# Optimization experiments

Hardware: AMD Instinct MI355X
Metric: run time of the kernel (lower is better)

Reference implementation:

```python
import jax, jax.numpy as jnp
import numpy as np

B, H, W = 4, 1024, 1024

# 8-tap Sobel-style stencil: offsets in (u, v) units of (dx, dy)
OFF_U = jnp.array([-1.0, -1.0, -1.0, 0.0, 0.0, 1.0, 1.0, 1.0], dtype=jnp.float32)
OFF_V = jnp.array([-1.0, 0.0, 1.0, -1.0, 1.0, -1.0, 0.0, 1.0], dtype=jnp.float32)
KU = jnp.array([-0.25, -0.5, -0.25, 0.0, 0.0, 0.25, 0.5, 0.25], dtype=jnp.float32)
KV = jnp.array([-0.25, 0.0, 0.25, -0.5, 0.5, -0.25, 0.0, 0.25], dtype=jnp.float32)


def setup_inputs() -> dict:
    key = jax.random.key(0)
    k1, k2 = jax.random.split(key)
    x = jax.random.uniform(k1, (B, 3, H, W), dtype=jnp.float32)
    sigma = jax.random.uniform(k2, (B,), dtype=jnp.float32) * 2.0 + 0.5  # pixels
    return {"x": x, "sigma": sigma}


def _bilinear(tex, u, v):
    # tex: [3, H, W]; u, v: [8, H, W] normalized UV in [0,1]
    Hh, Ww = tex.shape[1], tex.shape[2]
    px = u * Ww - 0.5
    py = v * Hh - 0.5
    x0 = jnp.floor(px)
    y0 = jnp.floor(py)
    fx = (px - x0)[None]  # [1,8,H,W]
    fy = (py - y0)[None]
    x0i = jnp.clip(x0.astype(jnp.int32), 0, Ww - 1)
    x1i = jnp.clip(x0i + 1, 0, Ww - 1)
    y0i = jnp.clip(y0.astype(jnp.int32), 0, Hh - 1)
    y1i = jnp.clip(y0i + 1, 0, Hh - 1)
    t00 = tex[:, y0i, x0i]  # [3,8,H,W]
    t01 = tex[:, y0i, x1i]
    t10 = tex[:, y1i, x0i]
    t11 = tex[:, y1i, x1i]
    return (t00 * (1 - fx) * (1 - fy) + t01 * fx * (1 - fy)
            + t10 * (1 - fx) * fy + t11 * fx * fy)


def reference(x, sigma):
    Bb, C, Hh, Ww = x.shape
    ys, xs = jnp.meshgrid(jnp.arange(Hh, dtype=x.dtype),
                          jnp.arange(Ww, dtype=x.dtype), indexing='ij')
    u0 = (xs + 0.5) / Ww  # pixel-center UV
    v0 = (ys + 0.5) / Hh
    dx = sigma / Ww  # [B]
    dy = sigma / Hh
    u = u0[None, None] + OFF_U[None, :, None, None] * dx[:, None, None, None]  # [B,8,H,W]
    v = v0[None, None] + OFF_V[None, :, None, None] * dy[:, None, None, None]
    s = jax.vmap(_bilinear)(x, u, v)  # [B,3,8,H,W]
    s_u = jnp.einsum('bcthw,t->bchw', s, KU)
    s_v = jnp.einsum('bcthw,t->bchw', s, KV)
    lum = jnp.array([100.0, 1.0, 1.0], dtype=x.dtype)[None, :, None, None]
    s_u = s_u * lum
    s_v = s_v * lum
    # structure tensor components E, G, F
    return jnp.stack([(s_u * s_u).sum(1), (s_v * s_v).sum(1), (s_u * s_v).sum(1)], axis=1)
```

## Files before the change

### kernel.cpp

```cpp
#include <hip/hip_runtime.h>


#define W_ 1024
#define H_ 1024
#define PLANE (1 << 20)
#define TCOLS 256
#define TROWS 8
#define ROWS 8
#define LSTRIDE 264
#define GPR 66

__device__ __forceinline__ float lerp1(float a, float b, float f) {
    return fmaf(f, b - a, a);
}

__device__ __forceinline__ void async_copy16(const float* g, float* s) {
    __builtin_amdgcn_global_load_lds(
        (const __attribute__((address_space(1))) unsigned int*)g,
        (__attribute__((address_space(3))) unsigned int*)s,
        16, 0, 0);
}

__device__ void slow_pixel(const float* __restrict__ Xb, float* __restrict__ Ob,
                           float sg, int xi, int y)
{
    float imf = floorf(-sg), ipf = floorf(sg);
    float fm  = -sg - imf;
    float fp  =  sg - ipf;
    int   im  = (int)imf, ip = (int)ipf;

    int cm0 = min(max(xi + im, 0), W_ - 1), cm1 = min(cm0 + 1, W_ - 1);
    int cp0 = min(max(xi + ip, 0), W_ - 1), cp1 = min(cp0 + 1, W_ - 1);
    int rm0 = min(max(y + im, 0), H_ - 1),  rm1 = min(rm0 + 1, H_ - 1);
    int rp0 = min(max(y + ip, 0), H_ - 1),  rp1 = min(rp0 + 1, H_ - 1);

    int o_rm0 = rm0 << 10, o_rm1 = rm1 << 10;
    int o_rp0 = rp0 << 10, o_rp1 = rp1 << 10;
    int o_r0  = y   << 10;

    float oxx = 0.f, oyy = 0.f, oxy = 0.f;

    #pragma unroll
    for (int c = 0; c < 3; ++c) {
        const float* base = Xb + ((size_t)c << 20);

        float hm_m0 = lerp1(base[o_rm0 + cm0], base[o_rm0 + cm1], fm);
        float hm_m1 = lerp1(base[o_rm1 + cm0], base[o_rm1 + cm1], fm);
        float hm_0  = lerp1(base[o_r0  + cm0], base[o_r0  + cm1], fm);
        float hm_p0 = lerp1(base[o_rp0 + cm0], base[o_rp0 + cm1], fm);
        float hm_p1 = lerp1(base[o_rp1 + cm0], base[o_rp1 + cm1], fm);
        float hp_m0 = lerp1(base[o_rm0 + cp0], base[o_rm0 + cp1], fp);
        float hp_m1 = lerp1(base[o_rm1 + cp0], base[o_rm1 + cp1], fp);
        float hp_0  = lerp1(base[o_r0  + cp0], base[o_r0  + cp1], fp);
        float hp_p0 = lerp1(base[o_rp0 + cp0], base[o_rp0 + cp1], fp);
        float hp_p1 = lerp1(base[o_rp1 + cp0], base[o_rp1 + cp1], fp);
        float h0_m0 = base[o_rm0 + xi], h0_m1 = base[o_rm1 + xi];
        float h0_p0 = base[o_rp0 + xi], h0_p1 = base[o_rp1 + xi];

        float t0 = lerp1(hm_m0, hm_m1, fm);
        float t1 = hm_0;
        float t2 = lerp1(hm_p0, hm_p1, fp);
        float t3 = lerp1(h0_m0, h0_m1, fm);
        float t4 = lerp1(h0_p0, h0_p1, fp);
        float t5 = lerp1(hp_m0, hp_m1, fm);
        float t6 = hp_0;
        float t7 = lerp1(hp_p0, hp_p1, fp);

        float su = 0.25f * (t5 + t7 - t0 - t2) + 0.5f * (t6 - t1);
        float sv = 0.25f * (t2 + t7 - t0 - t5) + 0.5f * (t4 - t3);

        float l2 = (c == 0) ? 10000.f : 1.f;
        oxx = fmaf(l2 * su, su, oxx);
        oyy = fmaf(l2 * sv, sv, oyy);
        oxy = fmaf(l2 * su, sv, oxy);
    }

    int pix = (y << 10) | xi;
    Ob[pix]             = oxx;
    Ob[PLANE + pix]     = oyy;
    Ob[2 * PLANE + pix] = oxy;
}

template<int N>
__device__ __forceinline__ void acc(float (&arr)[N], int k, float val) {
    if (k >= 0 && k < N) arr[k] += val;
}

template<int IP>
__device__ void fast_tile(const float* __restrict__ Xb, float* __restrict__ Ob,
                          float fp, float fm, int x0, int y0,
                          int tx, float* smem)
{
    constexpr int LROWS  = TROWS + 2 * IP + 2;
    constexpr int RW     = ROWS + 2 * IP + 2;
    constexpr int NG     = 3 * LROWS * GPR;
    constexpr int FULLIT = NG / 256;

    int x = x0 + tx;

    auto stage = [&](int g) {
        int row  = g / GPR;
        int grp  = g - row * GPR;
        int c    = row / LROWS;
        int lrow = row - c * LROWS;
        int gr   = min(max(y0 - IP - 1 + lrow, 0), H_ - 1);
        int gc   = min(max(x0 - 4 + grp * 4, 0), W_ - 4);
        async_copy16(Xb + ((size_t)c << 20) + (gr << 10) + gc,
                     smem + g * 4);
    };

    #pragma unroll
    for (int it = 0; it < FULLIT; ++it)
        stage(it * 256 + tx);
    if (FULLIT * 256 + tx < NG)
        stage(FULLIT * 256 + tx);

    __syncthreads();

    float oxx[ROWS], oyy[ROWS], oxy[ROWS];
    #pragma unroll
    for (int k = 0; k < ROWS; ++k) { oxx[k] = 0.f; oyy[k] = 0.f; oxy[k] = 0.f; }

    const float* spb = smem + tx + (3 - IP);

    #pragma unroll
    for (int c = 0; c < 3; ++c) {
        const float* sp = spb + c * (LROWS * LSTRIDE);

        float su[ROWS], sv[ROWS];
        #pragma unroll
        for (int k = 0; k < ROWS; ++k) { su[k] = 0.f; sv[k] = 0.f; }

        #pragma unroll
        for (int w = 0; w < RW; ++w) {
            float a0 = sp[w * LSTRIDE];
            float a1 = sp[w * LSTRIDE + 1];
            float cc = sp[w * LSTRIDE + IP + 1];
            float b0 = sp[w * LSTRIDE + 2 * IP + 1];
            float b1 = sp[w * LSTRIDE + 2 * IP + 2];
            float hm = lerp1(a0, a1, fm);
            float hp = lerp1(b0, b1, fp);
            float q  = hp - hm;
            float A  = 0.25f * q;
            float hq = 0.5f  * q;
            float Bv = fmaf(0.25f, hm + hp, 0.5f * cc);
            float fpA = fp * A,  fmA = fm * A;
            float fpB = fp * Bv, fmB = fm * Bv;

            acc(su, w,              fpA);
            acc(su, w - 1,          fmA);
            acc(su, w - IP - 1,     hq);
            acc(su, w - 2*IP - 1,   fmA);
            acc(su, w - 2*IP - 2,   fpA);
            acc(sv, w,             -fpB);
            acc(sv, w - 1,         -fmB);
            acc(sv, w - 2*IP - 1,   fmB);
            acc(sv, w - 2*IP - 2,   fpB);
        }

        float l2 = (c == 0) ? 10000.f : 1.f;
        #pragma unroll
        for (int k = 0; k < ROWS; ++k) {
            oxx[k] = fmaf(l2 * su[k], su[k], oxx[k]);
            oyy[k] = fmaf(l2 * sv[k], sv[k], oyy[k]);
            oxy[k] = fmaf(l2 * su[k], sv[k], oxy[k]);
        }
    }

    bool okx = (x > IP) && (x < W_ - 1 - IP);
    #pragma unroll
    for (int k = 0; k < ROWS; ++k) {
        int y = y0 + k;
        if (okx && y > IP) {
            int pix = (y << 10) | x;
            Ob[pix]             = oxx[k];
            Ob[PLANE + pix]     = oyy[k];
            Ob[2 * PLANE + pix] = oxy[k];
        }
    }
}

__global__ __launch_bounds__(256) void st_kernel(
    const float* __restrict__ X, const float* __restrict__ S,
    float* __restrict__ O)
{
    int b  = blockIdx.z;
    const float* Xb = X + (size_t)b * 3 * PLANE;
    float*       Ob = O + (size_t)b * 3 * PLANE;
    float sg = S[b];

    int tx = threadIdx.x;

    if (blockIdx.y == 0) {
        int t = blockIdx.x * 256 + tx;
        #pragma unroll
        for (int it = 0; it < 9; ++it) {
            int pidx = t + it * 1024;
            if (pidx < 6144) {
                int yy = pidx / 6;
                int cc = pidx - yy * 6;
                int xx = (cc < 3) ? cc : (W_ - 6 + cc);
                slow_pixel(Xb, Ob, sg, xx, yy);
            } else if (pidx < 9216) {
                int p2 = pidx - 6144;
                slow_pixel(Xb, Ob, sg, p2 & 1023, p2 >> 10);
            }
        }
        return;
    }

    int x0 = blockIdx.x * TCOLS;
    int y0 = (blockIdx.y - 1) * TROWS;

    int ipv = (int)floorf(sg);
    int imv = (int)floorf(-sg);
    bool sig_ok = (imv == -ipv - 1) && ipv >= 0 && ipv <= 2;
    float fp = sg - (float)ipv;
    float fm = 1.0f - fp;

    __shared__ float smem[3 * (TROWS + 6) * LSTRIDE];

    if (sig_ok) {
        switch (ipv) {
            case 0:  fast_tile<0>(Xb, Ob, fp, fm, x0, y0, tx, smem); break;
            case 1:  fast_tile<1>(Xb, Ob, fp, fm, x0, y0, tx, smem); break;
            default: fast_tile<2>(Xb, Ob, fp, fm, x0, y0, tx, smem); break;
        }
    } else {
        for (int k = 0; k < ROWS; ++k)
            slow_pixel(Xb, Ob, sg, x0 + tx, y0 + k);
    }
}

extern "C" void kernel_launch(void* const* d_in, const int* in_sizes, int n_in,
                              void* d_out, int out_size, void* d_ws, size_t ws_size,
                              hipStream_t stream) {
    const float* x     = (const float*)d_in[0];
    const float* sigma = (const float*)d_in[1];
    float* out = (float*)d_out;

    dim3 grid(W_ / TCOLS, H_ / TROWS + 1, 4), block(256, 1);
    hipLaunchKernelGGL(st_kernel, grid, block, 0, stream, x, sigma, out);
}
```

Baseline: 131.1 us.

## Widen tiles to two pixels per thread and stage channels one at a time

Each thread now computes two adjacent output columns, sharing shared-memory loads between neighbouring taps. The tile grows to 512 columns. Shared memory now holds one channel at a time, loaded and synchronised per channel, which cuts LDS footprint but serialises load and compute. Outputs are written as float2 pairs. Border-pixel work is spread over four block rows instead of one.

Measured after the change: 124.1 us. 5.3% less time.

```diff
diff --git a/kernel.cpp b/kernel.cpp
--- a/kernel.cpp
+++ b/kernel.cpp
@@ -4,11 +4,11 @@
 #define W_ 1024
 #define H_ 1024
 #define PLANE (1 << 20)
-#define TCOLS 256
+#define TCOLS 512
 #define TROWS 8
 #define ROWS 8
-#define LSTRIDE 264
-#define GPR 66
+#define LSTRIDE 520
+#define GPR 130
 
 __device__ __forceinline__ float lerp1(float a, float b, float f) {
     return fmaf(f, b - a, a);
@@ -93,89 +93,113 @@
 {
     constexpr int LROWS  = TROWS + 2 * IP + 2;
     constexpr int RW     = ROWS + 2 * IP + 2;
-    constexpr int NG     = 3 * LROWS * GPR;
+    constexpr int NG     = LROWS * GPR;
     constexpr int FULLIT = NG / 256;
-
-    int x = x0 + tx;
-
-    auto stage = [&](int g) {
-        int row  = g / GPR;
-        int grp  = g - row * GPR;
-        int c    = row / LROWS;
-        int lrow = row - c * LROWS;
-        int gr   = min(max(y0 - IP - 1 + lrow, 0), H_ - 1);
-        int gc   = min(max(x0 - 4 + grp * 4, 0), W_ - 4);
-        async_copy16(Xb + ((size_t)c << 20) + (gr << 10) + gc,
-                     smem + g * 4);
-    };
-
-    #pragma unroll
-    for (int it = 0; it < FULLIT; ++it)
-        stage(it * 256 + tx);
-    if (FULLIT * 256 + tx < NG)
-        stage(FULLIT * 256 + tx);
-
-    __syncthreads();
-
-    float oxx[ROWS], oyy[ROWS], oxy[ROWS];
-    #pragma unroll
-    for (int k = 0; k < ROWS; ++k) { oxx[k] = 0.f; oyy[k] = 0.f; oxy[k] = 0.f; }
-
-    const float* spb = smem + tx + (3 - IP);
+    constexpr int NT     = 2 * IP + 4;
+
+    float oxx[2][ROWS], oyy[2][ROWS], oxy[2][ROWS];
+    #pragma unroll
+    for (int l = 0; l < 2; ++l)
+        #pragma unroll
+        for (int k = 0; k < ROWS; ++k) { oxx[l][k] = 0.f; oyy[l][k] = 0.f; oxy[l][k] = 0.f; }
+
+    const float* sp = smem + 2 * tx + 4 - IP - 1;
 
     #pragma unroll
     for (int c = 0; c < 3; ++c) {
-        const float* sp = spb + c * (LROWS * LSTRIDE);
-
-        float su[ROWS], sv[ROWS];
-        #pragma unroll
-        for (int k = 0; k < ROWS; ++k) { su[k] = 0.f; sv[k] = 0.f; }
+        const float* Xc = Xb + ((size_t)c << 20);
+
+        #pragma unroll
+        for (int it = 0; it < FULLIT; ++it) {
+            int g   = it * 256 + tx;
+            int row = g / GPR;
+            int grp = g - row * GPR;
+            int gr  = min(max(y0 - IP - 1 + row, 0), H_ - 1);
+            int gc  = min(max(x0 - 4 + grp * 4, 0), W_ - 4);
+            async_copy16(Xc + (gr << 10) + gc, smem + g * 4);
+        }
+        {
+            int g = FULLIT * 256 + tx;
+            if (g < NG) {
+                int row = g / GPR;
+                int grp = g - row * GPR;
+                int gr  = min(max(y0 - IP - 1 + row, 0), H_ - 1);
+                int gc  = min(max(x0 - 4 + grp * 4, 0), W_ - 4);
+                async_copy16(Xc + (gr << 10) + gc, smem + g * 4);
+            }
+        }
+        __syncthreads();
+
+        float su[2][ROWS], sv[2][ROWS];
+        #pragma unroll
+        for (int l = 0; l < 2; ++l)
+            #pragma unroll
+            for (int k = 0; k < ROWS; ++k) { su[l][k] = 0.f; sv[l][k] = 0.f; }
 
         #pragma unroll
         for (int w = 0; w < RW; ++w) {
-            float a0 = sp[w * LSTRIDE];
-            float a1 = sp[w * LSTRIDE + 1];
-            float cc = sp[w * LSTRIDE + IP + 1];
-            float b0 = sp[w * LSTRIDE + 2 * IP + 1];
-            float b1 = sp[w * LSTRIDE + 2 * IP + 2];
-            float hm = lerp1(a0, a1, fm);
-            float hp = lerp1(b0, b1, fp);
-            float q  = hp - hm;
-            float A  = 0.25f * q;
-            float hq = 0.5f  * q;
-            float Bv = fmaf(0.25f, hm + hp, 0.5f * cc);
-            float fpA = fp * A,  fmA = fm * A;
-            float fpB = fp * Bv, fmB = fm * Bv;
-
-            acc(su, w,              fpA);
-            acc(su, w - 1,          fmA);
-            acc(su, w - IP - 1,     hq);
-            acc(su, w - 2*IP - 1,   fmA);
-            acc(su, w - 2*IP - 2,   fpA);
-            acc(sv, w,             -fpB);
-            acc(sv, w - 1,         -fmB);
-            acc(sv, w - 2*IP - 1,   fmB);
-            acc(sv, w - 2*IP - 2,   fpB);
+            float v[NT];
+            #pragma unroll
+            for (int j = 0; j < NT; ++j) v[j] = sp[w * LSTRIDE + j];
+
+            #pragma unroll
+            for (int l = 0; l < 2; ++l) {
+                float hm = lerp1(v[l],            v[l + 1],        fm);
+                float hp = lerp1(v[2*IP + 1 + l], v[2*IP + 2 + l], fp);
+                float cc = v[IP + 1 + l];
+                float q  = hp - hm;
+                float A  = 0.25f * q;
+                float hq = 0.5f  * q;
+                float Bv = fmaf(0.25f, hm + hp, 0.5f * cc);
+                float fpA = fp * A,  fmA = fm * A;
+                float fpB = fp * Bv, fmB = fm * Bv;
+
+                acc(su[l], w,              fpA);
+                acc(su[l], w - 1,          fmA);
+                acc(su[l], w - IP - 1,     hq);
+                acc(su[l], w - 2*IP - 1,   fmA);
+                acc(su[l], w - 2*IP - 2,   fpA);
+                acc(sv[l], w,             -fpB);
+                acc(sv[l], w - 1,         -fmB);
+                acc(sv[l], w - 2*IP - 1,   fmB);
+                acc(sv[l], w - 2*IP - 2,   fpB);
+            }
         }
 
         float l2 = (c == 0) ? 10000.f : 1.f;
         #pragma unroll
-        for (int k = 0; k < ROWS; ++k) {
-            oxx[k] = fmaf(l2 * su[k], su[k], oxx[k]);
-            oyy[k] = fmaf(l2 * sv[k], sv[k], oyy[k]);
-            oxy[k] = fmaf(l2 * su[k], sv[k], oxy[k]);
-        }
-    }
-
-    bool okx = (x > IP) && (x < W_ - 1 - IP);
+        for (int l = 0; l < 2; ++l)
+            #pragma unroll
+            for (int k = 0; k < ROWS; ++k) {
+                oxx[l][k] = fmaf(l2 * su[l][k], su[l][k], oxx[l][k]);
+                oyy[l][k] = fmaf(l2 * sv[l][k], sv[l][k], oyy[l][k]);
+                oxy[l][k] = fmaf(l2 * su[l][k], sv[l][k], oxy[l][k]);
+            }
+
+        __syncthreads();
+    }
+
+    int xg = x0 + 2 * tx;
+    bool ok0 = (xg     > IP) && (xg     < W_ - 1 - IP);
+    bool ok1 = (xg + 1 > IP) && (xg + 1 < W_ - 1 - IP);
     #pragma unroll
     for (int k = 0; k < ROWS; ++k) {
         int y = y0 + k;
-        if (okx && y > IP) {
-            int pix = (y << 10) | x;
-            Ob[pix]             = oxx[k];
-            Ob[PLANE + pix]     = oyy[k];
-            Ob[2 * PLANE + pix] = oxy[k];
+        if (y <= IP) continue;
+        int pix = (y << 10) + xg;
+        float vals[3][2] = {{oxx[0][k], oxx[1][k]},
+                            {oyy[0][k], oyy[1][k]},
+                            {oxy[0][k], oxy[1][k]}};
+        #pragma unroll
+        for (int p = 0; p < 3; ++p) {
+            float* dst = Ob + (size_t)p * PLANE + pix;
+            if (ok0 && ok1) {
+                *reinterpret_cast<float2*>(dst) =
+                    make_float2(vals[p][0], vals[p][1]);
+            } else {
+                if (ok0) dst[0] = vals[p][0];
+                if (ok1) dst[1] = vals[p][1];
+            }
         }
     }
 }
@@ -191,11 +215,11 @@
 
     int tx = threadIdx.x;
 
-    if (blockIdx.y == 0) {
-        int t = blockIdx.x * 256 + tx;
-        #pragma unroll
-        for (int it = 0; it < 9; ++it) {
-            int pidx = t + it * 1024;
+    if (blockIdx.y < 4) {
+        int t = (blockIdx.y * gridDim.x + blockIdx.x) * 256 + tx;
+        #pragma unroll
+        for (int it = 0; it < 5; ++it) {
+            int pidx = t + it * 2048;
             if (pidx < 6144) {
                 int yy = pidx / 6;
                 int cc = pidx - yy * 6;
@@ -210,7 +234,7 @@
     }
 
     int x0 = blockIdx.x * TCOLS;
-    int y0 = (blockIdx.y - 1) * TROWS;
+    int y0 = (blockIdx.y - 4) * TROWS;
 
     int ipv = (int)floorf(sg);
     int imv = (int)floorf(-sg);
@@ -218,7 +242,7 @@
     float fp = sg - (float)ipv;
     float fm = 1.0f - fp;
 
-    __shared__ float smem[3 * (TROWS + 6) * LSTRIDE];
+    __shared__ __align__(16) float smem[(TROWS + 6) * LSTRIDE];
 
     if (sig_ok) {
         switch (ipv) {
@@ -227,8 +251,10 @@
             default: fast_tile<2>(Xb, Ob, fp, fm, x0, y0, tx, smem); break;
         }
     } else {
-        for (int k = 0; k < ROWS; ++k)
-            slow_pixel(Xb, Ob, sg, x0 + tx, y0 + k);
+        #pragma unroll
+        for (int l = 0; l < 2; ++l)
+            for (int k = 0; k < ROWS; ++k)
+                slow_pixel(Xb, Ob, sg, x0 + 2 * tx + l, y0 + k);
     }
 }
 
@@ -239,6 +265,6 @@
     const float* sigma = (const float*)d_in[1];
     float* out = (float*)d_out;
 
-    dim3 grid(W_ / TCOLS, H_ / TROWS + 1, 4), block(256, 1);
+    dim3 grid(W_ / TCOLS, H_ / TROWS + 4, 4), block(256, 1);
     hipLaunchKernelGGL(st_kernel, grid, block, 0, stream, x, sigma, out);
 }
```
